# Optimization experiments

Hardware: AMD Instinct MI355X
Metric: run time of the kernel (lower is better)

Reference implementation:

```python
import jax, jax.numpy as jnp
import numpy as np

N = 50000   # nodes
E = 500000  # edges
B = 50      # graphs
H, D = 4, 64
NEG = 0.2   # leaky_relu slope in GATv2


def setup_inputs() -> dict:
    key = jax.random.key(0)
    ks = iter(jax.random.split(key, 40))
    rn = lambda shape, s=0.1: jax.random.normal(next(ks), shape, jnp.float32) * s
    inp = {
        'x': rn((N, 8), 1.0),
        'edge_index': jax.random.randint(next(ks), (2, E), 0, N, jnp.int64),
        'edge_attr': rn((E, 1), 1.0),
        'batch': jnp.sort(jax.random.randint(next(ks), (N,), 0, B, jnp.int64)),
        'enc_w': rn((8, 64)), 'enc_b': rn((64,)),
        'g1_wl': rn((64, 256)), 'g1_bl': rn((256,)),
        'g1_wr': rn((64, 256)), 'g1_br': rn((256,)),
        'g1_we': rn((1, 256)), 'g1_att': rn((H, D)), 'g1_bias': rn((256,)),
        'g2_wl': rn((256, 256)), 'g2_bl': rn((256,)),
        'g2_wr': rn((256, 256)), 'g2_br': rn((256,)),
        'g2_we': rn((1, 256)), 'g2_att': rn((H, D)), 'g2_bias': rn((256,)),
        'p1_w': rn((256, 128)), 'p1_b': rn((128,)),
        'ln_g': jnp.ones((128,), jnp.float32), 'ln_b': jnp.zeros((128,), jnp.float32),
        'p2_w': rn((128, 64)), 'p2_b': rn((64,)),
        'hc_w': rn((64, 1)), 'hc_b': rn((1,)),
        'hf_w': rn((64, 9)), 'hf_b': rn((9,)),
    }
    return inp


def gatv2(x, src, dst, ea, wl, bl, wr, br, we, att, bias):
    # x: [N, Fin]; src/dst: [E']; ea: [E',1]
    xl = (x @ wl + bl).reshape(N, H, D)  # source transform (lin_l)
    xr = (x @ wr + br).reshape(N, H, D)  # target transform (lin_r)
    e = (ea @ we).reshape(-1, H, D)      # edge embedding
    m = jax.nn.leaky_relu(xl[src] + xr[dst] + e, NEG)      # [E',H,D]
    logits = jnp.einsum('ehd,hd->eh', m, att)              # [E',H]
    # segment softmax over incoming edges of each target node
    lmax = jax.ops.segment_max(logits, dst, num_segments=N)
    lmax = jnp.where(jnp.isfinite(lmax), lmax, 0.0)
    ex = jnp.exp(logits - lmax[dst])
    den = jax.ops.segment_sum(ex, dst, num_segments=N)
    alpha = ex / den[dst]                                  # every node has a self-loop -> den > 0
    agg = jax.ops.segment_sum(xl[src] * alpha[:, :, None], dst, num_segments=N)
    return agg.reshape(N, H * D) + bias


def reference(x, edge_index, edge_attr, batch,
              enc_w, enc_b,
              g1_wl, g1_bl, g1_wr, g1_br, g1_we, g1_att, g1_bias,
              g2_wl, g2_bl, g2_wr, g2_br, g2_we, g2_att, g2_bias,
              p1_w, p1_b, ln_g, ln_b, p2_w, p2_b,
              hc_w, hc_b, hf_w, hf_b):
    # add self-loops once (PyG GATv2Conv default, edge_attr fill_value='mean')
    loop = jnp.arange(N, dtype=edge_index.dtype)
    src = jnp.concatenate([edge_index[0], loop])
    dst = jnp.concatenate([edge_index[1], loop])
    ea = jnp.concatenate([edge_attr,
                          jnp.broadcast_to(edge_attr.mean(0, keepdims=True), (N, 1))])

    h = jax.nn.relu(x @ enc_w + enc_b)
    h = jax.nn.relu(gatv2(h, src, dst, ea, g1_wl, g1_bl, g1_wr, g1_br, g1_we, g1_att, g1_bias))
    h = jax.nn.relu(gatv2(h, src, dst, ea, g2_wl, g2_bl, g2_wr, g2_br, g2_we, g2_att, g2_bias))

    # global mean pool over graphs
    sums = jax.ops.segment_sum(h, batch, num_segments=B)
    cnts = jax.ops.segment_sum(jnp.ones((N, 1), h.dtype), batch, num_segments=B)
    pooled = sums / jnp.maximum(cnts, 1.0)

    # post MLP: Linear -> LayerNorm -> ReLU -> (Dropout, eval=identity) -> Linear -> ReLU
    t = pooled @ p1_w + p1_b
    mu = t.mean(-1, keepdims=True)
    var = ((t - mu) ** 2).mean(-1, keepdims=True)
    t = (t - mu) / jnp.sqrt(var + 1e-5) * ln_g + ln_b
    t = jax.nn.relu(t)
    z = jax.nn.relu(t @ p2_w + p2_b)

    logit_cooling = (z @ hc_w + hc_b)[:, 0]
    logit_fatigue = z @ hf_w + hf_b
    return logit_cooling, logit_fatigue, z
```

## Files before the change

kernel.cpp:

```cpp
#include <hip/hip_runtime.h>
#include <hip/hip_bf16.h>

#define NN 50000
#define NE 500000
#define EP (NE + NN)
#define NB 50
#define NEG 0.2f
#define NBKT 196
#define CAP 3584
#define CHUNK 2048
#define NBLK1 ((EP + CHUNK - 1) / CHUNK)
#define NTILES 1563
#define GEMM_GX 392
#define SELF_FLAG (1 << 24)
#define SMEM_BYTES 31760

#define MEAN_BLKS 256
#define ENC_BLKS 12500
#define WCONV_BLKS 640
#define ZERO_BLKS 51
#define SETUP_GRID (NBLK1 + MEAN_BLKS + ENC_BLKS + WCONV_BLKS + 1 + ZERO_BLKS)

typedef __attribute__((ext_vector_type(8))) short short8;
typedef __attribute__((ext_vector_type(4))) float f32x4;

__device__ __forceinline__ ushort f2bf(float f) {
  unsigned u = __float_as_uint(f);
  unsigned r = (u + 0x7FFFu + ((u >> 16) & 1u)) >> 16;
  return (ushort)r;
}
__device__ __forceinline__ float bf2f(ushort b) {
  return __uint_as_float(((unsigned)b) << 16);
}

__device__ __forceinline__ float exp2s(float x) {
  float r;
  asm("v_exp_f32 %0, %1\ns_nop 0" : "=v"(r) : "v"(x));
  return r;
}

__device__ __forceinline__ float row_reduce16(float x) {
  x += __int_as_float(__builtin_amdgcn_mov_dpp(__float_as_int(x), 0xB1, 0xF, 0xF, true));
  x += __int_as_float(__builtin_amdgcn_mov_dpp(__float_as_int(x), 0x4E, 0xF, 0xF, true));
  x += __int_as_float(__builtin_amdgcn_mov_dpp(__float_as_int(x), 0x124, 0xF, 0xF, true));
  x += __int_as_float(__builtin_amdgcn_mov_dpp(__float_as_int(x), 0x128, 0xF, 0xF, true));
  return x;
}

__global__ __launch_bounds__(256) void setup_kernel(
    const float* __restrict__ x, const float* __restrict__ enc_w,
    const float* __restrict__ enc_b, ushort* __restrict__ h0,
    const float* __restrict__ ea, float* __restrict__ partials,
    const int* __restrict__ ei, int* __restrict__ gcursor,
    int2* __restrict__ bucketed,
    const float* __restrict__ g1_wl, const float* __restrict__ g1_wr,
    const float* __restrict__ g2_wl, const float* __restrict__ g2_wr,
    ushort* __restrict__ w1l, ushort* __restrict__ w1r,
    ushort* __restrict__ w2l, ushort* __restrict__ w2r,
    const float* __restrict__ att1, const float* __restrict__ att2,
    float* __restrict__ a06_1, float* __restrict__ a04_1,
    float* __restrict__ a06_2, float* __restrict__ a04_2,
    float* __restrict__ zero_region) {
  __shared__ float sw[4];
  __shared__ int hist[NBKT];
  __shared__ int lbase[NBKT];
  int b = blockIdx.x, t = threadIdx.x;
  if (b < NBLK1) {
    int e0 = b * CHUNK;
    for (int i = t; i < NBKT; i += 256) hist[i] = 0;
    __syncthreads();
    int packed[8], eab[8], bkt[8];
#pragma unroll
    for (int j = 0; j < 8; j++) {
      int e = e0 + j * 256 + t;
      bool valid = e < EP;
      int src, dst, fl = 0;
      float v = 0.f;
      if (e < NE) {
        src = ei[e];
        dst = ei[NE + e];
        v = ea[e];
      } else {
        int n = valid ? (e - NE) : 0;
        src = dst = n;
        fl = SELF_FLAG;
      }
      bkt[j] = valid ? (dst >> 8) : -1;
      packed[j] = src | ((dst & 255) << 16) | fl;
      eab[j] = __float_as_int(v);
      if (valid) atomicAdd(&hist[dst >> 8], 1);
    }
    __syncthreads();
    for (int i = t; i < NBKT; i += 256)
      lbase[i] = hist[i] ? (i * CAP + atomicAdd(&gcursor[i], hist[i])) : 0;
    __syncthreads();
#pragma unroll
    for (int j = 0; j < 8; j++) {
      if (bkt[j] >= 0) {
        int pos = atomicAdd(&lbase[bkt[j]], 1);
        pos = min(pos, (bkt[j] + 1) * CAP - 1);
        bucketed[pos] = make_int2(packed[j], eab[j]);
      }
    }
    return;
  }
  b -= NBLK1;
  if (b < MEAN_BLKS) {
    int idx = b * 256 + t;
    float v = 0.f;
    for (int i = idx; i < NE; i += 65536) v += ea[i];
    for (int off = 1; off < 64; off <<= 1) v += __shfl_xor(v, off, 64);
    if ((t & 63) == 0) sw[t >> 6] = v;
    __syncthreads();
    if (t == 0) partials[b] = sw[0] + sw[1] + sw[2] + sw[3];
    return;
  }
  b -= MEAN_BLKS;
  if (b < ENC_BLKS) {
    int i = b * 256 + t;
    int n = i >> 6, j = i & 63;
    float acc = enc_b[j];
#pragma unroll
    for (int k = 0; k < 8; k++) acc += x[n * 8 + k] * enc_w[k * 64 + j];
    h0[i] = f2bf(fmaxf(acc, 0.f));
    return;
  }
  b -= ENC_BLKS;
  if (b < WCONV_BLKS) {
    if (b < 128) {
      int sec = b >> 6;
      const float* W = sec ? g1_wr : g1_wl;
      ushort* Wt = sec ? w1r : w1l;
      int i = (b & 63) * 256 + t;
      int n = i >> 6, k = i & 63;
      Wt[i] = f2bf(W[(size_t)k * 256 + n]);
    } else {
      int bb = b - 128;
      int sec = bb >> 8;
      const float* W = sec ? g2_wr : g2_wl;
      ushort* Wt = sec ? w2r : w2l;
      int i = (bb & 255) * 256 + t;
      int n = i >> 8, k = i & 255;
      Wt[i] = f2bf(W[(size_t)k * 256 + n]);
    }
    return;
  }
  b -= WCONV_BLKS;
  if (b == 0) {
    const float L2E = 1.44269504f;
    float v1 = att1[t], v2 = att2[t];
    a06_1[t] = 0.6f * L2E * v1;
    a04_1[t] = 0.4f * L2E * v1;
    a06_2[t] = 0.6f * L2E * v2;
    a04_2[t] = 0.4f * L2E * v2;
    return;
  }
  b -= 1;
  {
    int i = b * 256 + t;
    if (i < NB * 256 + NB) zero_region[i] = 0.f;
  }
}

template <int K, bool WITH_SORT>
__global__ __launch_bounds__(256) void dual_linear_pb(
    const ushort* __restrict__ A, const ushort* __restrict__ Wl,
    const ushort* __restrict__ Wr, const float* __restrict__ bl,
    const float* __restrict__ br, ushort* __restrict__ xl,
    ushort* __restrict__ xr,
    const int* __restrict__ gcursor, const float* __restrict__ partials,
    const int2* __restrict__ bucketed, int2* __restrict__ sedge,
    int* __restrict__ offsets, int* __restrict__ counts) {
  __shared__ __align__(16) char smem[SMEM_BYTES];
  int t = threadIdx.x;
  if (WITH_SORT && blockIdx.x >= GEMM_GX) {
    if (blockIdx.y != 0) return;
    int2* stage = (int2*)smem;
    int* hist = (int*)(smem + CAP * 8);
    int* scn = hist + 256;
    int* cur = scn + 256;
    float* sw = (float*)(cur + 256);
    int b = blockIdx.x - GEMM_GX;
    float pv = partials[t];
    for (int off = 1; off < 64; off <<= 1) pv += __shfl_xor(pv, off, 64);
    if ((t & 63) == 0) sw[t >> 6] = pv;
    hist[t] = 0;
    __syncthreads();
    int meanb = __float_as_int((sw[0] + sw[1] + sw[2] + sw[3]) * (1.0f / NE));
    int base = b * CAP;
    int nb = min(gcursor[b], CAP - 16);
    for (int i = t; i < nb; i += 256) {
      int2 s = bucketed[base + i];
      if (s.x & SELF_FLAG) s.y = meanb;
      stage[i] = s;
    }
    __syncthreads();
    if (t < 16) {
      int2 pv2 = make_int2((stage[0].x & 0xFFFF) << 9, stage[0].y);
      sedge[base + nb + t] = pv2;
    }
    for (int i = t; i < nb; i += 256) atomicAdd(&hist[(stage[i].x >> 16) & 255], 1);
    __syncthreads();
    int v = hist[t];
    scn[t] = v;
    __syncthreads();
    for (int off = 1; off < 256; off <<= 1) {
      int add = (t >= off) ? scn[t - off] : 0;
      __syncthreads();
      scn[t] += add;
      __syncthreads();
    }
    int excl = scn[t] - v;
    cur[t] = excl;
    __syncthreads();
    for (int i = t; i < nb; i += 256) {
      int dl = (stage[i].x >> 16) & 255;
      int p = atomicAdd(&cur[dl], 1);
      sedge[base + p] = make_int2((stage[i].x & 0xFFFF) << 9, stage[i].y);
    }
    int d = b * 256 + t;
    if (d < NN) {
      offsets[d] = base + excl;
      counts[d] = v;
    }
    return;
  }
  ushort(*lt)[272] = reinterpret_cast<ushort(*)[272]>(smem);
  int wave = t >> 6, lane = t & 63;
  int lr = lane & 15;
  int kb = (lane >> 4) * 8;
  const ushort* W = blockIdx.y ? Wr : Wl;
  const float* bias = blockIdx.y ? br : bl;
  ushort* O = blockIdx.y ? xr : xl;
  const int c0 = wave * 64;
  const ushort* pb = W + (size_t)(c0 + lr) * K + kb;
  int cb = (t & 31) * 8;

  for (int tt = blockIdx.x; tt < NTILES; tt += GEMM_GX) {
    int r = tt * 32;
    int ra0 = min(r + lr, NN - 1);
    int ra1 = min(r + 16 + lr, NN - 1);
    const ushort* pa0 = A + (size_t)ra0 * K + kb;
    const ushort* pa1 = A + (size_t)ra1 * K + kb;
    f32x4 acc[2][4];
#pragma unroll
    for (int fr = 0; fr < 2; fr++)
#pragma unroll
      for (int fc = 0; fc < 4; fc++) acc[fr][fc] = (f32x4){0.f, 0.f, 0.f, 0.f};
#pragma unroll
    for (int kc = 0; kc < K; kc += 64) {
      short8 a00 = *(const short8*)(pa0 + kc);
      short8 a01 = *(const short8*)(pa0 + kc + 32);
      short8 a10 = *(const short8*)(pa1 + kc);
      short8 a11 = *(const short8*)(pa1 + kc + 32);
      short8 b0[4], b1[4];
#pragma unroll
      for (int fc = 0; fc < 4; fc++) {
        b0[fc] = *(const short8*)(pb + (size_t)fc * 16 * K + kc);
        b1[fc] = *(const short8*)(pb + (size_t)fc * 16 * K + kc + 32);
      }
#pragma unroll
      for (int fc = 0; fc < 4; fc++) {
        acc[0][fc] = __builtin_amdgcn_mfma_f32_16x16x32_bf16(a00, b0[fc], acc[0][fc], 0, 0, 0);
        acc[1][fc] = __builtin_amdgcn_mfma_f32_16x16x32_bf16(a10, b0[fc], acc[1][fc], 0, 0, 0);
      }
#pragma unroll
      for (int fc = 0; fc < 4; fc++) {
        acc[0][fc] = __builtin_amdgcn_mfma_f32_16x16x32_bf16(a01, b1[fc], acc[0][fc], 0, 0, 0);
        acc[1][fc] = __builtin_amdgcn_mfma_f32_16x16x32_bf16(a11, b1[fc], acc[1][fc], 0, 0, 0);
      }
    }
#pragma unroll
    for (int fc = 0; fc < 4; fc++) {
      int c = c0 + fc * 16 + lr;
      float bv = bias[c];
#pragma unroll
      for (int fr = 0; fr < 2; fr++) {
#pragma unroll
        for (int j = 0; j < 4; j++) {
          int row = fr * 16 + (lane >> 4) * 4 + j;
          int cs = c ^ (((row >> 2) & 3) << 4);
          lt[row][cs] = f2bf(acc[fr][fc][j] + bv);
        }
      }
    }
    __syncthreads();
#pragma unroll
    for (int it = 0; it < 4; it++) {
      int rl = (t >> 5) + it * 8;
      int row = r + rl;
      if (row < NN) {
        int cs = cb ^ (((rl >> 2) & 3) << 4);
        short8 v = *(const short8*)&lt[rl][cs];
        *(short8*)(O + (size_t)row * 256 + cb) = v;
      }
    }
    __syncthreads();
  }
}

__global__ __launch_bounds__(256) void gat_fused_kernel(const int* __restrict__ offsets,
                                                        const int* __restrict__ counts,
                                                        const int2* __restrict__ sedge,
                                                        const ushort* __restrict__ xl,
                                                        const ushort* __restrict__ xr,
                                                        const float* __restrict__ we,
                                                        const float* __restrict__ a06p,
                                                        const float* __restrict__ a04p,
                                                        const float* __restrict__ bias,
                                                        ushort* __restrict__ hb) {
  int w = threadIdx.x >> 6, lane = threadIdx.x & 63;
  int d = blockIdx.x * 4 + w;
  if (d >= NN) return;
  int off = offsets[d], cnt = counts[d];
  const int c4 = lane * 4;
  ushort4 xru = *(const ushort4*)(xr + (size_t)d * 256 + c4);
  const float4 xr4 = {bf2f(xru.x), bf2f(xru.y), bf2f(xru.z), bf2f(xru.w)};
  const float4 we4 = *(const float4*)(we + c4);
  const float4 a06 = *(const float4*)(a06p + c4);
  const float4 a04 = *(const float4*)(a04p + c4);
  float4 acc = {0.f, 0.f, 0.f, 0.f};
  float den = 0.f;
  const int2* pe = sedge + off;
  const char* xlc = (const char*)xl + (size_t)c4 * 2;
  int2 e0 = pe[0], e1 = pe[1], e2 = pe[2], e3 = pe[3];
  ushort4 xu0 = *(const ushort4*)(xlc + (size_t)(unsigned)e0.x);
  ushort4 xu1 = *(const ushort4*)(xlc + (size_t)(unsigned)e1.x);
  ushort4 xu2 = *(const ushort4*)(xlc + (size_t)(unsigned)e2.x);
  ushort4 xu3 = *(const ushort4*)(xlc + (size_t)(unsigned)e3.x);
  int2 f0 = pe[4], f1 = pe[5], f2 = pe[6], f3 = pe[7];
  ushort4 yu0 = *(const ushort4*)(xlc + (size_t)(unsigned)f0.x);
  ushort4 yu1 = *(const ushort4*)(xlc + (size_t)(unsigned)f1.x);
  ushort4 yu2 = *(const ushort4*)(xlc + (size_t)(unsigned)f2.x);
  ushort4 yu3 = *(const ushort4*)(xlc + (size_t)(unsigned)f3.x);
#pragma unroll 2
  for (int i = 0; i < cnt; i += 4) {
    float ce0 = __int_as_float(e0.y), ce1 = __int_as_float(e1.y);
    float ce2 = __int_as_float(e2.y), ce3 = __int_as_float(e3.y);
    float4 x0 = {bf2f(xu0.x), bf2f(xu0.y), bf2f(xu0.z), bf2f(xu0.w)};
    float4 x1 = {bf2f(xu1.x), bf2f(xu1.y), bf2f(xu1.z), bf2f(xu1.w)};
    float4 x2 = {bf2f(xu2.x), bf2f(xu2.y), bf2f(xu2.z), bf2f(xu2.w)};
    float4 x3 = {bf2f(xu3.x), bf2f(xu3.y), bf2f(xu3.z), bf2f(xu3.w)};
    e0 = f0; e1 = f1; e2 = f2; e3 = f3;
    xu0 = yu0; xu1 = yu1; xu2 = yu2; xu3 = yu3;
    f0 = pe[i + 8]; f1 = pe[i + 9]; f2 = pe[i + 10]; f3 = pe[i + 11];
    yu0 = *(const ushort4*)(xlc + (size_t)(unsigned)f0.x);
    yu1 = *(const ushort4*)(xlc + (size_t)(unsigned)f1.x);
    yu2 = *(const ushort4*)(xlc + (size_t)(unsigned)f2.x);
    yu3 = *(const ushort4*)(xlc + (size_t)(unsigned)f3.x);
    float v0, v1, v2, v3;
    float p0, p1, p2, p3;
    v0 = x0.x + fmaf(ce0, we4.x, xr4.x);
    v1 = x0.y + fmaf(ce0, we4.y, xr4.y);
    v2 = x0.z + fmaf(ce0, we4.z, xr4.z);
    v3 = x0.w + fmaf(ce0, we4.w, xr4.w);
    p0 = fmaf(a06.x, v0, a04.x * fabsf(v0));
    p0 = fmaf(a06.y, v1, fmaf(a04.y, fabsf(v1), p0));
    p0 = fmaf(a06.z, v2, fmaf(a04.z, fabsf(v2), p0));
    p0 = fmaf(a06.w, v3, fmaf(a04.w, fabsf(v3), p0));
    v0 = x1.x + fmaf(ce1, we4.x, xr4.x);
    v1 = x1.y + fmaf(ce1, we4.y, xr4.y);
    v2 = x1.z + fmaf(ce1, we4.z, xr4.z);
    v3 = x1.w + fmaf(ce1, we4.w, xr4.w);
    p1 = fmaf(a06.x, v0, a04.x * fabsf(v0));
    p1 = fmaf(a06.y, v1, fmaf(a04.y, fabsf(v1), p1));
    p1 = fmaf(a06.z, v2, fmaf(a04.z, fabsf(v2), p1));
    p1 = fmaf(a06.w, v3, fmaf(a04.w, fabsf(v3), p1));
    v0 = x2.x + fmaf(ce2, we4.x, xr4.x);
    v1 = x2.y + fmaf(ce2, we4.y, xr4.y);
    v2 = x2.z + fmaf(ce2, we4.z, xr4.z);
    v3 = x2.w + fmaf(ce2, we4.w, xr4.w);
    p2 = fmaf(a06.x, v0, a04.x * fabsf(v0));
    p2 = fmaf(a06.y, v1, fmaf(a04.y, fabsf(v1), p2));
    p2 = fmaf(a06.z, v2, fmaf(a04.z, fabsf(v2), p2));
    p2 = fmaf(a06.w, v3, fmaf(a04.w, fabsf(v3), p2));
    v0 = x3.x + fmaf(ce3, we4.x, xr4.x);
    v1 = x3.y + fmaf(ce3, we4.y, xr4.y);
    v2 = x3.z + fmaf(ce3, we4.z, xr4.z);
    v3 = x3.w + fmaf(ce3, we4.w, xr4.w);
    p3 = fmaf(a06.x, v0, a04.x * fabsf(v0));
    p3 = fmaf(a06.y, v1, fmaf(a04.y, fabsf(v1), p3));
    p3 = fmaf(a06.z, v2, fmaf(a04.z, fabsf(v2), p3));
    p3 = fmaf(a06.w, v3, fmaf(a04.w, fabsf(v3), p3));
    p0 = row_reduce16(p0);
    p1 = row_reduce16(p1);
    p2 = row_reduce16(p2);
    p3 = row_reduce16(p3);
    float ex0 = exp2s(fminf(p0, 120.f));
    float ex1 = exp2s(fminf(p1, 120.f));
    float ex2 = exp2s(fminf(p2, 120.f));
    float ex3 = exp2s(fminf(p3, 120.f));
    ex1 = (i + 1 < cnt) ? ex1 : 0.f;
    ex2 = (i + 2 < cnt) ? ex2 : 0.f;
    ex3 = (i + 3 < cnt) ? ex3 : 0.f;
    den += (ex0 + ex1) + (ex2 + ex3);
    acc.x = fmaf(x0.x, ex0, fmaf(x1.x, ex1, fmaf(x2.x, ex2, fmaf(x3.x, ex3, acc.x))));
    acc.y = fmaf(x0.y, ex0, fmaf(x1.y, ex1, fmaf(x2.y, ex2, fmaf(x3.y, ex3, acc.y))));
    acc.z = fmaf(x0.z, ex0, fmaf(x1.z, ex1, fmaf(x2.z, ex2, fmaf(x3.z, ex3, acc.z))));
    acc.w = fmaf(x0.w, ex0, fmaf(x1.w, ex1, fmaf(x2.w, ex2, fmaf(x3.w, ex3, acc.w))));
  }
  const float4 b4 = *(const float4*)(bias + c4);
  float inv = 1.f / den;
  ushort4 o;
  o.x = f2bf(fmaxf(fmaf(acc.x, inv, b4.x), 0.f));
  o.y = f2bf(fmaxf(fmaf(acc.y, inv, b4.y), 0.f));
  o.z = f2bf(fmaxf(fmaf(acc.z, inv, b4.z), 0.f));
  o.w = f2bf(fmaxf(fmaf(acc.w, inv, b4.w), 0.f));
  *(ushort4*)(hb + (size_t)d * 256 + c4) = o;
}

__global__ __launch_bounds__(256) void pool_kernel(const ushort* __restrict__ h,
                                                   const int* __restrict__ batch,
                                                   float* __restrict__ sums,
                                                   float* __restrict__ cnts) {
  __shared__ int sb[128];
  int n0 = blockIdx.x * 128;
  int j = threadIdx.x;
  int count = min(128, NN - n0);
  if (count <= 0) return;
  for (int t = threadIdx.x; t < count; t += 256) sb[t] = batch[n0 + t];
  __syncthreads();
  float acc = 0.f;
  int run = 0;
  int cur = sb[0];
  for (int i = 0; i < count; ++i) {
    int b = sb[i];
    if (b != cur) {
      atomicAdd(&sums[(size_t)cur * 256 + j], acc);
      if (j == 0) atomicAdd(&cnts[cur], (float)run);
      acc = 0.f;
      run = 0;
      cur = b;
    }
    acc += bf2f(h[(size_t)(n0 + i) * 256 + j]);
    run++;
  }
  atomicAdd(&sums[(size_t)cur * 256 + j], acc);
  if (j == 0) atomicAdd(&cnts[cur], (float)run);
}

__global__ __launch_bounds__(128) void head_kernel(const float* __restrict__ sums,
                                                   const float* __restrict__ cnts,
                                                   const float* __restrict__ p1_w,
                                                   const float* __restrict__ p1_b,
                                                   const float* __restrict__ ln_g,
                                                   const float* __restrict__ ln_b,
                                                   const float* __restrict__ p2_w,
                                                   const float* __restrict__ p2_b,
                                                   const float* __restrict__ hc_w,
                                                   const float* __restrict__ hc_b,
                                                   const float* __restrict__ hf_w,
                                                   const float* __restrict__ hf_b,
                                                   float* __restrict__ out) {
  int g = blockIdx.x;
  int j = threadIdx.x;
  __shared__ float sp[256], st[128], sz[64];
  float cnt = fmaxf(cnts[g], 1.0f);
  for (int t = j; t < 256; t += 128) sp[t] = sums[(size_t)g * 256 + t] / cnt;
  __syncthreads();
  float acc = p1_b[j];
  for (int k = 0; k < 256; k++) acc += sp[k] * p1_w[(size_t)k * 128 + j];
  st[j] = acc;
  __syncthreads();
  float mu = 0.f;
  for (int k = 0; k < 128; k++) mu += st[k];
  mu *= (1.f / 128.f);
  float var = 0.f;
  for (int k = 0; k < 128; k++) {
    float d = st[k] - mu;
    var += d * d;
  }
  var *= (1.f / 128.f);
  float tj = (acc - mu) * rsqrtf(var + 1e-5f) * ln_g[j] + ln_b[j];
  tj = fmaxf(tj, 0.f);
  __syncthreads();
  st[j] = tj;
  __syncthreads();
  if (j < 64) {
    float z = p2_b[j];
    for (int k = 0; k < 128; k++) z += st[k] * p2_w[(size_t)k * 64 + j];
    z = fmaxf(z, 0.f);
    sz[j] = z;
    out[500 + (size_t)g * 64 + j] = z;
  }
  __syncthreads();
  if (j == 0) {
    float c = hc_b[0];
    for (int k = 0; k < 64; k++) c += sz[k] * hc_w[k];
    out[g] = c;
  }
  if (j >= 1 && j < 10) {
    int f = j - 1;
    float v = hf_b[f];
    for (int k = 0; k < 64; k++) v += sz[k] * hf_w[(size_t)k * 9 + f];
    out[50 + (size_t)g * 9 + f] = v;
  }
}

extern "C" void kernel_launch(void* const* d_in, const int* in_sizes, int n_in,
                              void* d_out, int out_size, void* d_ws, size_t ws_size,
                              hipStream_t stream) {
  const float* x = (const float*)d_in[0];
  const int* ei = (const int*)d_in[1];
  const float* ea = (const float*)d_in[2];
  const int* batch = (const int*)d_in[3];
  const float* enc_w = (const float*)d_in[4];
  const float* enc_b = (const float*)d_in[5];
  const float* g1_wl = (const float*)d_in[6];
  const float* g1_bl = (const float*)d_in[7];
  const float* g1_wr = (const float*)d_in[8];
  const float* g1_br = (const float*)d_in[9];
  const float* g1_we = (const float*)d_in[10];
  const float* g1_att = (const float*)d_in[11];
  const float* g1_bias = (const float*)d_in[12];
  const float* g2_wl = (const float*)d_in[13];
  const float* g2_bl = (const float*)d_in[14];
  const float* g2_wr = (const float*)d_in[15];
  const float* g2_br = (const float*)d_in[16];
  const float* g2_we = (const float*)d_in[17];
  const float* g2_att = (const float*)d_in[18];
  const float* g2_bias = (const float*)d_in[19];
  const float* p1_w = (const float*)d_in[20];
  const float* p1_b = (const float*)d_in[21];
  const float* ln_g = (const float*)d_in[22];
  const float* ln_b = (const float*)d_in[23];
  const float* p2_w = (const float*)d_in[24];
  const float* p2_b = (const float*)d_in[25];
  const float* hc_w = (const float*)d_in[26];
  const float* hc_b = (const float*)d_in[27];
  const float* hf_w = (const float*)d_in[28];
  const float* hf_b = (const float*)d_in[29];
  float* out = (float*)d_out;

  ushort* xlb = (ushort*)d_ws;
  ushort* xrb = xlb + (size_t)NN * 256;
  ushort* hb = xrb + (size_t)NN * 256;
  ushort* h0b = hb + (size_t)NN * 256;
  ushort* w1l = h0b + (size_t)NN * 64;
  ushort* w1r = w1l + 256 * 64;
  ushort* w2l = w1r + 256 * 64;
  ushort* w2r = w2l + 256 * 256;
  int2* bucketed = (int2*)(w2r + 256 * 256);
  int2* sedge = bucketed + (size_t)NBKT * CAP;
  int* gcursor = (int*)(sedge + (size_t)NBKT * CAP);
  int* counts = gcursor + NBKT;
  int* offsets = counts + NN;
  float* sums = (float*)(offsets + NN);
  float* cnts = sums + (size_t)NB * 256;
  float* partials = cnts + NB;
  float* a06_1 = partials + 256;
  float* a04_1 = a06_1 + 256;
  float* a06_2 = a04_1 + 256;
  float* a04_2 = a06_2 + 256;

  hipMemsetAsync(gcursor, 0, NBKT * sizeof(int), stream);

  setup_kernel<<<SETUP_GRID, 256, 0, stream>>>(
      x, enc_w, enc_b, h0b, ea, partials, ei, gcursor, bucketed,
      g1_wl, g1_wr, g2_wl, g2_wr, w1l, w1r, w2l, w2r,
      g1_att, g2_att, a06_1, a04_1, a06_2, a04_2, sums);

  const int nGatBlocks = (NN + 3) / 4;

  dim3 g64(GEMM_GX + NBKT, 2);
  dual_linear_pb<64, true><<<g64, 256, 0, stream>>>(
      h0b, w1l, w1r, g1_bl, g1_br, xlb, xrb,
      gcursor, partials, bucketed, sedge, offsets, counts);
  gat_fused_kernel<<<nGatBlocks, 256, 0, stream>>>(offsets, counts, sedge, xlb, xrb,
                                                   g1_we, a06_1, a04_1, g1_bias, hb);

  dim3 g256(GEMM_GX, 2);
  dual_linear_pb<256, false><<<g256, 256, 0, stream>>>(
      hb, w2l, w2r, g2_bl, g2_br, xlb, xrb,
      gcursor, partials, bucketed, sedge, offsets, counts);
  gat_fused_kernel<<<nGatBlocks, 256, 0, stream>>>(offsets, counts, sedge, xlb, xrb,
                                                   g2_we, a06_2, a04_2, g2_bias, hb);

  pool_kernel<<<(NN + 127) / 128, 256, 0, stream>>>(hb, batch, sums, cnts);
  head_kernel<<<NB, 128, 0, stream>>>(sums, cnts, p1_w, p1_b, ln_g, ln_b, p2_w, p2_b,
                                      hc_w, hc_b, hf_w, hf_b, out);
}
```

Baseline: 242.9 us.

## Double-buffer A tiles in LDS with async global-to-LDS loads in dual GEMM

The dual linear GEMM now stages each 32-row A tile into a double-buffered, XOR-swizzled LDS region using global_load_lds. The next tile's load is issued before computing the current one, so global latency can overlap with the MFMA work. Fragments are then read from LDS instead of directly from global memory. This enlarges shared memory per block, especially for K=256, which can lower occupancy. It also drops the row clamp, so the final tile may read past the last valid row of A.

```diff
diff --git a/kernel.cpp b/kernel.cpp
--- a/kernel.cpp
+++ b/kernel.cpp
@@ -13,7 +13,7 @@
 #define NTILES 1563
 #define GEMM_GX 392
 #define SELF_FLAG (1 << 24)
-#define SMEM_BYTES 31760
+#define SORT_SMEM 31760
 
 #define MEAN_BLKS 256
 #define ENC_BLKS 12500
@@ -171,7 +171,11 @@
     const int* __restrict__ gcursor, const float* __restrict__ partials,
     const int2* __restrict__ bucketed, int2* __restrict__ sedge,
     int* __restrict__ offsets, int* __restrict__ counts) {
-  __shared__ __align__(16) char smem[SMEM_BYTES];
+  constexpr int C16 = K / 8;
+  constexpr int ABUF_USH = 32 * K;
+  constexpr int GEMM_SMEM = 2 * ABUF_USH * 2 + 32 * 272 * 2;
+  constexpr int ARENA = (WITH_SORT && GEMM_SMEM < SORT_SMEM) ? SORT_SMEM : GEMM_SMEM;
+  __shared__ __align__(16) char smem[ARENA];
   int t = threadIdx.x;
   if (WITH_SORT && blockIdx.x >= GEMM_GX) {
     if (blockIdx.y != 0) return;
@@ -225,7 +229,8 @@
     }
     return;
   }
-  ushort(*lt)[272] = reinterpret_cast<ushort(*)[272]>(smem);
+  ushort* abuf = (ushort*)smem;
+  ushort(*lt)[272] = reinterpret_cast<ushort(*)[272]>(smem + (size_t)2 * ABUF_USH * 2);
   int wave = t >> 6, lane = t & 63;
   int lr = lane & 15;
   int kb = (lane >> 4) * 8;
@@ -236,12 +241,28 @@
   const ushort* pb = W + (size_t)(c0 + lr) * K + kb;
   int cb = (t & 31) * 8;
 
+  auto STAGE = [&](int bi, int rr) {
+#pragma unroll
+    for (int i = 0; i < K / 64; i++) {
+      int s = i * 256 + wave * 64 + lane;
+      int row = s / C16;
+      int colg = (s % C16) ^ (row & 7);
+      const ushort* g = A + (size_t)(rr + row) * K + colg * 8;
+      ushort* l = abuf + (size_t)bi * ABUF_USH + (size_t)(i * 256 + wave * 64) * 8;
+      __builtin_amdgcn_global_load_lds(
+          (const __attribute__((address_space(1))) unsigned*)g,
+          (__attribute__((address_space(3))) unsigned*)l, 16, 0, 0);
+    }
+  };
+
+  int cur = 0;
+  STAGE(0, blockIdx.x * 32);
+  __syncthreads();
   for (int tt = blockIdx.x; tt < NTILES; tt += GEMM_GX) {
+    int nxt = tt + GEMM_GX;
+    if (nxt < NTILES) STAGE(cur ^ 1, nxt * 32);
     int r = tt * 32;
-    int ra0 = min(r + lr, NN - 1);
-    int ra1 = min(r + 16 + lr, NN - 1);
-    const ushort* pa0 = A + (size_t)ra0 * K + kb;
-    const ushort* pa1 = A + (size_t)ra1 * K + kb;
+    const ushort* ab = abuf + (size_t)cur * ABUF_USH;
     f32x4 acc[2][4];
 #pragma unroll
     for (int fr = 0; fr < 2; fr++)
@@ -249,10 +270,13 @@
       for (int fc = 0; fc < 4; fc++) acc[fr][fc] = (f32x4){0.f, 0.f, 0.f, 0.f};
 #pragma unroll
     for (int kc = 0; kc < K; kc += 64) {
-      short8 a00 = *(const short8*)(pa0 + kc);
-      short8 a01 = *(const short8*)(pa0 + kc + 32);
-      short8 a10 = *(const short8*)(pa1 + kc);
-      short8 a11 = *(const short8*)(pa1 + kc + 32);
+      int c16a = (kb + kc) >> 3;
+      int c16b = (kb + kc + 32) >> 3;
+      int lr2 = lr + 16;
+      short8 a00 = *(const short8*)(ab + (size_t)(lr * C16 + (c16a ^ (lr & 7))) * 8);
+      short8 a01 = *(const short8*)(ab + (size_t)(lr * C16 + (c16b ^ (lr & 7))) * 8);
+      short8 a10 = *(const short8*)(ab + (size_t)(lr2 * C16 + (c16a ^ (lr2 & 7))) * 8);
+      short8 a11 = *(const short8*)(ab + (size_t)(lr2 * C16 + (c16b ^ (lr2 & 7))) * 8);
       short8 b0[4], b1[4];
 #pragma unroll
       for (int fc = 0; fc < 4; fc++) {
@@ -296,6 +320,7 @@
       }
     }
     __syncthreads();
+    cur ^= 1;
   }
 }
 
```

Result: faster. 225.3 us (-7.2%).
